# Performance work log

Measured on AMD Instinct MI355X. Metric: run time of the kernel, lower is better.

Reference implementation:

```python
import jax, jax.numpy as jnp
import numpy as np

N_INIT = jnp.array([17.047, 14.099, 3.625], dtype=jnp.float32)
CA_INIT = jnp.array([16.967, 12.784, 4.338], dtype=jnp.float32)
C_INIT = jnp.array([15.685, 12.755, 5.133], dtype=jnp.float32)


def _unit(x):
    return x / (jnp.linalg.norm(x, axis=-1, keepdims=True) + 1e-8)


def _place_dihedral(a, b, c, bond_angle, bond_length, torsion):
    # a,b,c: [B,3]; bond_angle/bond_length/torsion: [B]
    ab = b - a
    bc = _unit(c - b)
    cr = jnp.cross(ab, bc)
    crn = jnp.linalg.norm(cr, axis=-1, keepdims=True)
    n_main = _unit(cr)
    # collinear fallback (per-element; almost never triggers for real angles)
    perp = jnp.zeros_like(bc).at[..., 0].set(1.0)
    ct = jnp.cross(bc, perp)
    ctn = jnp.linalg.norm(ct, axis=-1, keepdims=True)
    perp2 = jnp.where(ctn < 1e-6, jnp.zeros_like(bc).at[..., 1].set(1.0), perp)
    n_fb = _unit(jnp.cross(bc, perp2))
    n = jnp.where(crn < 1e-6, n_fb, n_main)
    nbc = jnp.cross(n, bc)
    m = jnp.stack([bc, nbc, n], axis=-1)  # [B,3,3]
    d_local = jnp.stack([
        -bond_length * jnp.cos(bond_angle),
        bond_length * jnp.cos(torsion) * jnp.sin(bond_angle),
        bond_length * jnp.sin(torsion) * jnp.sin(bond_angle),
    ], axis=-1)  # [B,3]
    d = jnp.einsum('bij,bj->bi', m, d_local)
    return d + c


def _nerf_build(phi, psi, omega, bond_lengths, bond_angles):
    B, L = phi.shape
    init = jnp.broadcast_to(jnp.stack([N_INIT, CA_INIT, C_INIT]), (B, 3, 3))
    # per-step params, leading axis = residue index i in [0, L-2]
    xs = (
        psi[:, :L - 1].T,                 # psi_i
        omega[:, :L - 1].T,               # omega_i
        phi[:, 1:].T,                     # phi_{i+1}
        bond_lengths[:, :L - 1, 2].T,     # C-N length
        bond_lengths[:, :L - 1, 0].T,     # N-CA length
        bond_lengths[:, :L - 1, 1].T,     # CA-C length
        bond_angles[:, :L - 1, 1].T,      # CA-C-N angle
        bond_angles[:, :L - 1, 2].T,      # C-N-CA angle
        bond_angles[:, :L - 1, 0].T,      # N-CA-C angle
    )

    def step(prev, x):
        psi_i, omega_i, phi_i, len_cn, len_nca, len_cac, ang_cacn, ang_cnca, ang_ncac = x
        a, b, c = prev[:, 0], prev[:, 1], prev[:, 2]
        n = _place_dihedral(a, b, c, ang_cacn, len_cn, psi_i)
        ca = _place_dihedral(b, c, n, ang_cnca, len_nca, omega_i)
        cc = _place_dihedral(c, n, ca, ang_ncac, len_cac, phi_i)
        new = jnp.stack([n, ca, cc], axis=1)  # [B,3,3]
        return new, new

    _, outs = jax.lax.scan(step, init, xs)  # [L-1,B,3,3]
    rest = outs.transpose(1, 0, 2, 3).reshape(B, 3 * (L - 1), 3)
    return jnp.concatenate([init, rest], axis=1)  # [B, 3L, 3]


def setup_inputs() -> dict:
    key = jax.random.key(0)
    k0, k1, k2, k3, k4 = jax.random.split(key, 5)
    B, L = 4096, 512
    phi = jax.random.normal(k0, (B, L), dtype=jnp.float32)
    psi = jax.random.normal(k1, (B, L), dtype=jnp.float32)
    omega = jax.random.normal(k2, (B, L), dtype=jnp.float32)
    # realistic positive bond lengths (~1.0-1.5 A) and bond angles (~1.5-2.3 rad)
    bond_lengths = 1.0 + 0.5 * jax.random.uniform(k3, (B, L, 3), dtype=jnp.float32)
    bond_angles = 1.5 + 0.8 * jax.random.uniform(k4, (B, L, 3), dtype=jnp.float32)
    return {"phi": phi, "psi": psi, "omega": omega,
            "bond_lengths": bond_lengths, "bond_angles": bond_angles}


def reference(phi, psi, omega, bond_lengths, bond_angles):
    return _nerf_build(phi, psi, omega, bond_lengths, bond_angles)
```

## Files before the change

### kernel.cpp

```cpp
#include <hip/hip_runtime.h>
#include <math.h>


#define LCH 512
#define NRES 511
#define RPL 8

struct Xf { float r[9]; float t[3]; };

__device__ __forceinline__ Xf xf_compose(const Xf& A, const Xf& B) {
  Xf C;
#pragma unroll
  for (int i = 0; i < 3; ++i) {
    float a0 = A.r[3*i+0], a1 = A.r[3*i+1], a2 = A.r[3*i+2];
    C.r[3*i+0] = a0*B.r[0] + a1*B.r[3] + a2*B.r[6];
    C.r[3*i+1] = a0*B.r[1] + a1*B.r[4] + a2*B.r[7];
    C.r[3*i+2] = a0*B.r[2] + a1*B.r[5] + a2*B.r[8];
    C.t[i]     = a0*B.t[0] + a1*B.t[1] + a2*B.t[2] + A.t[i];
  }
  return C;
}

__device__ __forceinline__ void xf_step(Xf& P, float theta, float len, float tau) {
  float st, ct, sx, cx;
  __sincosf(theta, &st, &ct);
  __sincosf(tau, &sx, &cx);
  float ux = -ct, uy = cx*st, uz = sx*st;
  float v0 = -st, v1 = -ct*cx, v2 = -ct*sx;
  float c00 = P.r[0]*ux + P.r[1]*uy + P.r[2]*uz;
  float c10 = P.r[3]*ux + P.r[4]*uy + P.r[5]*uz;
  float c20 = P.r[6]*ux + P.r[7]*uy + P.r[8]*uz;
  float c01 = P.r[0]*v0 + P.r[1]*v1 + P.r[2]*v2;
  float c11 = P.r[3]*v0 + P.r[4]*v1 + P.r[5]*v2;
  float c21 = P.r[6]*v0 + P.r[7]*v1 + P.r[8]*v2;
  float c02 = P.r[2]*cx - P.r[1]*sx;
  float c12 = P.r[5]*cx - P.r[4]*sx;
  float c22 = P.r[8]*cx - P.r[7]*sx;
  P.t[0] += len*c00; P.t[1] += len*c10; P.t[2] += len*c20;
  P.r[0]=c00; P.r[1]=c01; P.r[2]=c02;
  P.r[3]=c10; P.r[4]=c11; P.r[5]=c12;
  P.r[6]=c20; P.r[7]=c21; P.r[8]=c22;
}

__device__ __forceinline__ void xf_set_delta(Xf& P, float theta, float len, float tau) {
  float st, ct, sx, cx;
  __sincosf(theta, &st, &ct);
  __sincosf(tau, &sx, &cx);
  float ux = -ct, uy = cx*st, uz = sx*st;
  P.r[0]=ux; P.r[1]=-st;    P.r[2]=0.f;
  P.r[3]=uy; P.r[4]=-ct*cx; P.r[5]=-sx;
  P.r[6]=uz; P.r[7]=-ct*sx; P.r[8]=cx;
  P.t[0]=len*ux; P.t[1]=len*uy; P.t[2]=len*uz;
}

__device__ __forceinline__ Xf xf_shfl_up(const Xf& P, int d) {
  Xf O;
#pragma unroll
  for (int i = 0; i < 9; ++i) O.r[i] = __shfl_up(P.r[i], d, 64);
#pragma unroll
  for (int i = 0; i < 3; ++i) O.t[i] = __shfl_up(P.t[i], d, 64);
  return O;
}

static __device__ const float c_init[9] = {
  17.047f, 14.099f, 3.625f,
  16.967f, 12.784f, 4.338f,
  15.685f, 12.755f, 5.133f };

__global__ __launch_bounds__(256) void nerf_wavescan_kernel(
    const float* __restrict__ g_phi, const float* __restrict__ g_psi,
    const float* __restrict__ g_omg, const float* __restrict__ g_bl,
    const float* __restrict__ g_ba, float* __restrict__ g_out)
{
  const int lane  = threadIdx.x & 63;
  const int wave  = threadIdx.x >> 6;
  const int chain = blockIdx.x * 4 + wave;

  const float* phir = g_phi + (size_t)chain * LCH;
  const float* psir = g_psi + (size_t)chain * LCH;
  const float* omgr = g_omg + (size_t)chain * LCH;
  const float* blr  = g_bl  + (size_t)chain * LCH * 3;
  const float* bar  = g_ba  + (size_t)chain * LCH * 3;

  const int j0 = lane * RPL;

  float psi_[RPL], omg_[RPL], phl_[RPL];
  float bl_[3*RPL], ba_[3*RPL];
  {
    const float4* p;
    p = (const float4*)(psir + j0);
#pragma unroll
    for (int q = 0; q < RPL/4; ++q) { float4 v = p[q];
      psi_[4*q]=v.x; psi_[4*q+1]=v.y; psi_[4*q+2]=v.z; psi_[4*q+3]=v.w; }
    p = (const float4*)(omgr + j0);
#pragma unroll
    for (int q = 0; q < RPL/4; ++q) { float4 v = p[q];
      omg_[4*q]=v.x; omg_[4*q+1]=v.y; omg_[4*q+2]=v.z; omg_[4*q+3]=v.w; }
    p = (const float4*)(phir + j0);
#pragma unroll
    for (int q = 0; q < RPL/4; ++q) { float4 v = p[q];
      phl_[4*q]=v.x; phl_[4*q+1]=v.y; phl_[4*q+2]=v.z; phl_[4*q+3]=v.w; }
    p = (const float4*)(blr + (size_t)j0*3);
#pragma unroll
    for (int q = 0; q < (3*RPL)/4; ++q) { float4 v = p[q];
      bl_[4*q]=v.x; bl_[4*q+1]=v.y; bl_[4*q+2]=v.z; bl_[4*q+3]=v.w; }
    p = (const float4*)(bar + (size_t)j0*3);
#pragma unroll
    for (int q = 0; q < (3*RPL)/4; ++q) { float4 v = p[q];
      ba_[4*q]=v.x; ba_[4*q+1]=v.y; ba_[4*q+2]=v.z; ba_[4*q+3]=v.w; }
  }
  float phi_next = __shfl_down(phl_[0], 1, 64);
  float phiN[RPL];
#pragma unroll
  for (int e = 0; e < RPL-1; ++e) phiN[e] = phl_[e+1];
  phiN[RPL-1] = phi_next;

  Xf P;
  xf_set_delta(P, ba_[1], bl_[2], psi_[0]);
  xf_step(P, ba_[2], bl_[0], omg_[0]);
  xf_step(P, ba_[0], bl_[1], phiN[0]);
#pragma unroll
  for (int e = 1; e < RPL; ++e) {
    if (j0 + e < NRES) {
      xf_step(P, ba_[3*e+1], bl_[3*e+2], psi_[e]);
      xf_step(P, ba_[3*e+2], bl_[3*e+0], omg_[e]);
      xf_step(P, ba_[3*e+0], bl_[3*e+1], phiN[e]);
    }
  }

#pragma unroll
  for (int d = 1; d < 64; d <<= 1) {
    Xf O = xf_shfl_up(P, d);
    if (lane >= d) P = xf_compose(O, P);
  }

  Xf E = xf_shfl_up(P, 1);
  Xf A;
  {
    const float ax=17.047f, ay=14.099f, az=3.625f;
    const float bx_=16.967f, by_=12.784f, bz_=4.338f;
    const float cx_=15.685f, cy_=12.755f, cz_=5.133f;
    float abx=bx_-ax, aby=by_-ay, abz=bz_-az;
    float vx=cx_-bx_, vy=cy_-by_, vz=cz_-bz_;
    float vn = sqrtf(vx*vx+vy*vy+vz*vz) + 1e-8f;
    vx/=vn; vy/=vn; vz/=vn;
    float crx = aby*vz - abz*vy;
    float cry = abz*vx - abx*vz;
    float crz = abx*vy - aby*vx;
    float cn = sqrtf(crx*crx+cry*cry+crz*crz) + 1e-8f;
    float nx=crx/cn, ny=cry/cn, nz=crz/cn;
    float mx = ny*vz - nz*vy;
    float my = nz*vx - nx*vz;
    float mz = nx*vy - ny*vx;
    Xf I0;
    I0.r[0]=vx; I0.r[1]=mx; I0.r[2]=nx;
    I0.r[3]=vy; I0.r[4]=my; I0.r[5]=ny;
    I0.r[6]=vz; I0.r[7]=mz; I0.r[8]=nz;
    I0.t[0]=cx_; I0.t[1]=cy_; I0.t[2]=cz_;
    A = (lane == 0) ? I0 : xf_compose(I0, E);
  }

  float* orow = g_out + (size_t)chain * (3*LCH) * 3;
  if (lane < 9) orow[lane] = c_init[lane];

#pragma unroll
  for (int e = 0; e < RPL; ++e) {
    int j = j0 + e;
    if (j < NRES) {
      float* o = orow + (size_t)(3 + 3*j) * 3;
      xf_step(A, ba_[3*e+1], bl_[3*e+2], psi_[e]);
      o[0]=A.t[0]; o[1]=A.t[1]; o[2]=A.t[2];
      xf_step(A, ba_[3*e+2], bl_[3*e+0], omg_[e]);
      o[3]=A.t[0]; o[4]=A.t[1]; o[5]=A.t[2];
      xf_step(A, ba_[3*e+0], bl_[3*e+1], phiN[e]);
      o[6]=A.t[0]; o[7]=A.t[1]; o[8]=A.t[2];
    }
  }
}

extern "C" void kernel_launch(void* const* d_in, const int* in_sizes, int n_in,
                              void* d_out, int out_size, void* d_ws, size_t ws_size,
                              hipStream_t stream) {
  const float* phi = (const float*)d_in[0];
  const float* psi = (const float*)d_in[1];
  const float* omg = (const float*)d_in[2];
  const float* bl  = (const float*)d_in[3];
  const float* ba  = (const float*)d_in[4];
  float* out = (float*)d_out;
  const int B = in_sizes[0] / LCH;
  hipLaunchKernelGGL(nerf_wavescan_kernel, dim3(B / 4), dim3(256), 0, stream,
                     phi, psi, omg, bl, ba, out);
}
```

Before: 171.5 us.

## Stage output in LDS for coalesced float4 stores; realign per-lane residue ownership

Each lane now owns output atoms 72*lane..72*lane+71 by shifting residue ownership by one, pulling the previous lane's last-residue params via shuffles, and dropping the tail bounds checks. Outputs are written to a padded per-wave shared-memory buffer (stride 73), then written back as fully coalesced float4 stores across the wave. This replaces the scattered strided 4-byte global stores. In exchange it adds LDS traffic, shuffles, some index arithmetic, and 73 KB of shared memory per block, which limits occupancy.

```diff
diff --git a/kernel.cpp b/kernel.cpp
--- a/kernel.cpp
+++ b/kernel.cpp
@@ -4,7 +4,6 @@
 
 #define LCH 512
 #define NRES 511
-#define RPL 8
 
 struct Xf { float r[9]; float t[3]; };
 
@@ -53,6 +52,13 @@
   P.t[0]=len*ux; P.t[1]=len*uy; P.t[2]=len*uz;
 }
 
+__device__ __forceinline__ void xf_identity(Xf& A) {
+  A.r[0]=1.f; A.r[1]=0.f; A.r[2]=0.f;
+  A.r[3]=0.f; A.r[4]=1.f; A.r[5]=0.f;
+  A.r[6]=0.f; A.r[7]=0.f; A.r[8]=1.f;
+  A.t[0]=0.f; A.t[1]=0.f; A.t[2]=0.f;
+}
+
 __device__ __forceinline__ Xf xf_shfl_up(const Xf& P, int d) {
   Xf O;
 #pragma unroll
@@ -62,19 +68,19 @@
   return O;
 }
 
-static __device__ const float c_init[9] = {
-  17.047f, 14.099f, 3.625f,
-  16.967f, 12.784f, 4.338f,
-  15.685f, 12.755f, 5.133f };
+#define LSTRIDE 73
 
 __global__ __launch_bounds__(256) void nerf_wavescan_kernel(
     const float* __restrict__ g_phi, const float* __restrict__ g_psi,
     const float* __restrict__ g_omg, const float* __restrict__ g_bl,
     const float* __restrict__ g_ba, float* __restrict__ g_out)
 {
+  __shared__ float S[4][LSTRIDE * 64];
+
   const int lane  = threadIdx.x & 63;
   const int wave  = threadIdx.x >> 6;
   const int chain = blockIdx.x * 4 + wave;
+  float* sw = &S[wave][0];
 
   const float* phir = g_phi + (size_t)chain * LCH;
   const float* psir = g_psi + (size_t)chain * LCH;
@@ -82,50 +88,52 @@
   const float* blr  = g_bl  + (size_t)chain * LCH * 3;
   const float* bar  = g_ba  + (size_t)chain * LCH * 3;
 
-  const int j0 = lane * RPL;
-
-  float psi_[RPL], omg_[RPL], phl_[RPL];
-  float bl_[3*RPL], ba_[3*RPL];
+  const int j0 = lane * 8;
+
+  float psi_[8], omg_[8], phl_[8], bl_[24], ba_[24];
   {
     const float4* p;
     p = (const float4*)(psir + j0);
 #pragma unroll
-    for (int q = 0; q < RPL/4; ++q) { float4 v = p[q];
+    for (int q = 0; q < 2; ++q) { float4 v = p[q];
       psi_[4*q]=v.x; psi_[4*q+1]=v.y; psi_[4*q+2]=v.z; psi_[4*q+3]=v.w; }
     p = (const float4*)(omgr + j0);
 #pragma unroll
-    for (int q = 0; q < RPL/4; ++q) { float4 v = p[q];
+    for (int q = 0; q < 2; ++q) { float4 v = p[q];
       omg_[4*q]=v.x; omg_[4*q+1]=v.y; omg_[4*q+2]=v.z; omg_[4*q+3]=v.w; }
     p = (const float4*)(phir + j0);
 #pragma unroll
-    for (int q = 0; q < RPL/4; ++q) { float4 v = p[q];
+    for (int q = 0; q < 2; ++q) { float4 v = p[q];
       phl_[4*q]=v.x; phl_[4*q+1]=v.y; phl_[4*q+2]=v.z; phl_[4*q+3]=v.w; }
     p = (const float4*)(blr + (size_t)j0*3);
 #pragma unroll
-    for (int q = 0; q < (3*RPL)/4; ++q) { float4 v = p[q];
+    for (int q = 0; q < 6; ++q) { float4 v = p[q];
       bl_[4*q]=v.x; bl_[4*q+1]=v.y; bl_[4*q+2]=v.z; bl_[4*q+3]=v.w; }
     p = (const float4*)(bar + (size_t)j0*3);
 #pragma unroll
-    for (int q = 0; q < (3*RPL)/4; ++q) { float4 v = p[q];
+    for (int q = 0; q < 6; ++q) { float4 v = p[q];
       ba_[4*q]=v.x; ba_[4*q+1]=v.y; ba_[4*q+2]=v.z; ba_[4*q+3]=v.w; }
   }
-  float phi_next = __shfl_down(phl_[0], 1, 64);
-  float phiN[RPL];
-#pragma unroll
-  for (int e = 0; e < RPL-1; ++e) phiN[e] = phl_[e+1];
-  phiN[RPL-1] = phi_next;
+
+  float psip = __shfl_up(psi_[7], 1, 64);
+  float omgp = __shfl_up(omg_[7], 1, 64);
+  float pbl0 = __shfl_up(bl_[21], 1, 64);
+  float pbl1 = __shfl_up(bl_[22], 1, 64);
+  float pbl2 = __shfl_up(bl_[23], 1, 64);
+  float pba0 = __shfl_up(ba_[21], 1, 64);
+  float pba1 = __shfl_up(ba_[22], 1, 64);
+  float pba2 = __shfl_up(ba_[23], 1, 64);
 
   Xf P;
-  xf_set_delta(P, ba_[1], bl_[2], psi_[0]);
-  xf_step(P, ba_[2], bl_[0], omg_[0]);
-  xf_step(P, ba_[0], bl_[1], phiN[0]);
-#pragma unroll
-  for (int e = 1; e < RPL; ++e) {
-    if (j0 + e < NRES) {
-      xf_step(P, ba_[3*e+1], bl_[3*e+2], psi_[e]);
-      xf_step(P, ba_[3*e+2], bl_[3*e+0], omg_[e]);
-      xf_step(P, ba_[3*e+0], bl_[3*e+1], phiN[e]);
-    }
+  xf_set_delta(P, pba1, pbl2, psip);
+  xf_step(P, pba2, pbl0, omgp);
+  xf_step(P, pba0, pbl1, phl_[0]);
+  if (lane == 0) xf_identity(P);
+#pragma unroll
+  for (int e = 0; e < 7; ++e) {
+    xf_step(P, ba_[3*e+1], bl_[3*e+2], psi_[e]);
+    xf_step(P, ba_[3*e+2], bl_[3*e+0], omg_[e]);
+    xf_step(P, ba_[3*e+0], bl_[3*e+1], phl_[e+1]);
   }
 
 #pragma unroll
@@ -160,21 +168,44 @@
     A = (lane == 0) ? I0 : xf_compose(I0, E);
   }
 
-  float* orow = g_out + (size_t)chain * (3*LCH) * 3;
-  if (lane < 9) orow[lane] = c_init[lane];
-
-#pragma unroll
-  for (int e = 0; e < RPL; ++e) {
-    int j = j0 + e;
-    if (j < NRES) {
-      float* o = orow + (size_t)(3 + 3*j) * 3;
-      xf_step(A, ba_[3*e+1], bl_[3*e+2], psi_[e]);
-      o[0]=A.t[0]; o[1]=A.t[1]; o[2]=A.t[2];
-      xf_step(A, ba_[3*e+2], bl_[3*e+0], omg_[e]);
-      o[3]=A.t[0]; o[4]=A.t[1]; o[5]=A.t[2];
-      xf_step(A, ba_[3*e+0], bl_[3*e+1], phiN[e]);
-      o[6]=A.t[0]; o[7]=A.t[1]; o[8]=A.t[2];
-    }
+  float* reg = sw + LSTRIDE * lane;
+  if (lane != 0) {
+    xf_step(A, pba1, pbl2, psip);
+    reg[0]=A.t[0]; reg[1]=A.t[1]; reg[2]=A.t[2];
+    xf_step(A, pba2, pbl0, omgp);
+    reg[3]=A.t[0]; reg[4]=A.t[1]; reg[5]=A.t[2];
+    xf_step(A, pba0, pbl1, phl_[0]);
+    reg[6]=A.t[0]; reg[7]=A.t[1]; reg[8]=A.t[2];
+  } else {
+    reg[0]=17.047f; reg[1]=14.099f; reg[2]=3.625f;
+    reg[3]=16.967f; reg[4]=12.784f; reg[5]=4.338f;
+    reg[6]=15.685f; reg[7]=12.755f; reg[8]=5.133f;
+  }
+#pragma unroll
+  for (int e = 0; e < 7; ++e) {
+    float* o = reg + 9 + 9*e;
+    xf_step(A, ba_[3*e+1], bl_[3*e+2], psi_[e]);
+    o[0]=A.t[0]; o[1]=A.t[1]; o[2]=A.t[2];
+    xf_step(A, ba_[3*e+2], bl_[3*e+0], omg_[e]);
+    o[3]=A.t[0]; o[4]=A.t[1]; o[5]=A.t[2];
+    xf_step(A, ba_[3*e+0], bl_[3*e+1], phl_[e+1]);
+    o[6]=A.t[0]; o[7]=A.t[1]; o[8]=A.t[2];
+  }
+
+  float* orow = g_out + (size_t)chain * (3 * LCH) * 3;
+  int g0 = 4 * lane;
+  int lo = g0 / 72;
+  int f  = g0 - 72 * lo;
+  int addr = LSTRIDE * lo + f;
+#pragma unroll
+  for (int q = 0; q < 18; ++q) {
+    float4 v;
+    v.x = sw[addr]; v.y = sw[addr+1]; v.z = sw[addr+2]; v.w = sw[addr+3];
+    *(float4*)(orow + 4*lane + 256*q) = v;
+    f += 40;
+    int wrap = (f >= 72) ? 1 : 0;
+    f -= 72 * wrap;
+    addr += 259 + wrap;
   }
 }
 
```

Result: faster. 167.1 us (-2.6%).

## Split each chain across a 256-thread block with two-level scan and LDS-staged output

Applied to the files above, without the earlier changes.

Each chain now gets a whole 256-thread block instead of one wave, so each thread handles two residues rather than eight. The per-wave transform totals are combined through shared memory. Outputs are staged in LDS and written back with coalesced stores instead of strided per-thread writes. This gives more parallelism and better store coalescing, at the cost of more compose work, block barriers, and less coalesced scalar input loads.

```diff
diff --git a/kernel.cpp b/kernel.cpp
--- a/kernel.cpp
+++ b/kernel.cpp
@@ -3,8 +3,6 @@
 
 
 #define LCH 512
-#define NRES 511
-#define RPL 8
 
 struct Xf { float r[9]; float t[3]; };
 
@@ -53,6 +51,13 @@
   P.t[0]=len*ux; P.t[1]=len*uy; P.t[2]=len*uz;
 }
 
+__device__ __forceinline__ void xf_identity(Xf& A) {
+  A.r[0]=1.f; A.r[1]=0.f; A.r[2]=0.f;
+  A.r[3]=0.f; A.r[4]=1.f; A.r[5]=0.f;
+  A.r[6]=0.f; A.r[7]=0.f; A.r[8]=1.f;
+  A.t[0]=0.f; A.t[1]=0.f; A.t[2]=0.f;
+}
+
 __device__ __forceinline__ Xf xf_shfl_up(const Xf& P, int d) {
   Xf O;
 #pragma unroll
@@ -62,19 +67,25 @@
   return O;
 }
 
-static __device__ const float c_init[9] = {
-  17.047f, 14.099f, 3.625f,
-  16.967f, 12.784f, 4.338f,
-  15.685f, 12.755f, 5.133f };
-
-__global__ __launch_bounds__(256) void nerf_wavescan_kernel(
+__device__ __forceinline__ void xf_load_lds(const float* p, Xf& A) {
+#pragma unroll
+  for (int i = 0; i < 9; ++i) A.r[i] = p[i];
+#pragma unroll
+  for (int i = 0; i < 3; ++i) A.t[i] = p[9+i];
+}
+
+__global__ __launch_bounds__(256) void nerf_r6_kernel(
     const float* __restrict__ g_phi, const float* __restrict__ g_psi,
     const float* __restrict__ g_omg, const float* __restrict__ g_bl,
     const float* __restrict__ g_ba, float* __restrict__ g_out)
 {
-  const int lane  = threadIdx.x & 63;
-  const int wave  = threadIdx.x >> 6;
-  const int chain = blockIdx.x * 4 + wave;
+  __shared__ float s_tot[48];
+  __shared__ float s_out[4608];
+
+  const int t    = threadIdx.x;
+  const int lane = t & 63;
+  const int wave = t >> 6;
+  const int chain = blockIdx.x;
 
   const float* phir = g_phi + (size_t)chain * LCH;
   const float* psir = g_psi + (size_t)chain * LCH;
@@ -82,51 +93,25 @@
   const float* blr  = g_bl  + (size_t)chain * LCH * 3;
   const float* bar  = g_ba  + (size_t)chain * LCH * 3;
 
-  const int j0 = lane * RPL;
-
-  float psi_[RPL], omg_[RPL], phl_[RPL];
-  float bl_[3*RPL], ba_[3*RPL];
-  {
-    const float4* p;
-    p = (const float4*)(psir + j0);
-#pragma unroll
-    for (int q = 0; q < RPL/4; ++q) { float4 v = p[q];
-      psi_[4*q]=v.x; psi_[4*q+1]=v.y; psi_[4*q+2]=v.z; psi_[4*q+3]=v.w; }
-    p = (const float4*)(omgr + j0);
-#pragma unroll
-    for (int q = 0; q < RPL/4; ++q) { float4 v = p[q];
-      omg_[4*q]=v.x; omg_[4*q+1]=v.y; omg_[4*q+2]=v.z; omg_[4*q+3]=v.w; }
-    p = (const float4*)(phir + j0);
-#pragma unroll
-    for (int q = 0; q < RPL/4; ++q) { float4 v = p[q];
-      phl_[4*q]=v.x; phl_[4*q+1]=v.y; phl_[4*q+2]=v.z; phl_[4*q+3]=v.w; }
-    p = (const float4*)(blr + (size_t)j0*3);
-#pragma unroll
-    for (int q = 0; q < (3*RPL)/4; ++q) { float4 v = p[q];
-      bl_[4*q]=v.x; bl_[4*q+1]=v.y; bl_[4*q+2]=v.z; bl_[4*q+3]=v.w; }
-    p = (const float4*)(bar + (size_t)j0*3);
-#pragma unroll
-    for (int q = 0; q < (3*RPL)/4; ++q) { float4 v = p[q];
-      ba_[4*q]=v.x; ba_[4*q+1]=v.y; ba_[4*q+2]=v.z; ba_[4*q+3]=v.w; }
-  }
-  float phi_next = __shfl_down(phl_[0], 1, 64);
-  float phiN[RPL];
-#pragma unroll
-  for (int e = 0; e < RPL-1; ++e) phiN[e] = phl_[e+1];
-  phiN[RPL-1] = phi_next;
+  const int jm = (2*t - 1) > 0 ? (2*t - 1) : 0;
+  const int jo = 2*t;
+
+  float psiA = psir[jm], psiB = psir[jo];
+  float omgA = omgr[jm], omgB = omgr[jo];
+  float phiA = phir[jo], phiB = phir[jo + 1];
+  float blA0 = blr[3*jm+0], blA1 = blr[3*jm+1], blA2 = blr[3*jm+2];
+  float blB0 = blr[3*jo+0], blB1 = blr[3*jo+1], blB2 = blr[3*jo+2];
+  float baA0 = bar[3*jm+0], baA1 = bar[3*jm+1], baA2 = bar[3*jm+2];
+  float baB0 = bar[3*jo+0], baB1 = bar[3*jo+1], baB2 = bar[3*jo+2];
 
   Xf P;
-  xf_set_delta(P, ba_[1], bl_[2], psi_[0]);
-  xf_step(P, ba_[2], bl_[0], omg_[0]);
-  xf_step(P, ba_[0], bl_[1], phiN[0]);
-#pragma unroll
-  for (int e = 1; e < RPL; ++e) {
-    if (j0 + e < NRES) {
-      xf_step(P, ba_[3*e+1], bl_[3*e+2], psi_[e]);
-      xf_step(P, ba_[3*e+2], bl_[3*e+0], omg_[e]);
-      xf_step(P, ba_[3*e+0], bl_[3*e+1], phiN[e]);
-    }
-  }
+  xf_set_delta(P, baA1, blA2, psiA);
+  xf_step(P, baA2, blA0, omgA);
+  xf_step(P, baA0, blA1, phiA);
+  if (t == 0) xf_identity(P);
+  xf_step(P, baB1, blB2, psiB);
+  xf_step(P, baB2, blB0, omgB);
+  xf_step(P, baB0, blB1, phiB);
 
 #pragma unroll
   for (int d = 1; d < 64; d <<= 1) {
@@ -134,7 +119,15 @@
     if (lane >= d) P = xf_compose(O, P);
   }
 
+  if (lane == 63) {
+#pragma unroll
+    for (int i = 0; i < 9; ++i) s_tot[12*wave + i] = P.r[i];
+#pragma unroll
+    for (int i = 0; i < 3; ++i) s_tot[12*wave + 9 + i] = P.t[i];
+  }
   Xf E = xf_shfl_up(P, 1);
+  __syncthreads();
+
   Xf A;
   {
     const float ax=17.047f, ay=14.099f, az=3.625f;
@@ -152,29 +145,45 @@
     float mx = ny*vz - nz*vy;
     float my = nz*vx - nx*vz;
     float mz = nx*vy - ny*vx;
-    Xf I0;
-    I0.r[0]=vx; I0.r[1]=mx; I0.r[2]=nx;
-    I0.r[3]=vy; I0.r[4]=my; I0.r[5]=ny;
-    I0.r[6]=vz; I0.r[7]=mz; I0.r[8]=nz;
-    I0.t[0]=cx_; I0.t[1]=cy_; I0.t[2]=cz_;
-    A = (lane == 0) ? I0 : xf_compose(I0, E);
-  }
-
-  float* orow = g_out + (size_t)chain * (3*LCH) * 3;
-  if (lane < 9) orow[lane] = c_init[lane];
-
-#pragma unroll
-  for (int e = 0; e < RPL; ++e) {
-    int j = j0 + e;
-    if (j < NRES) {
-      float* o = orow + (size_t)(3 + 3*j) * 3;
-      xf_step(A, ba_[3*e+1], bl_[3*e+2], psi_[e]);
-      o[0]=A.t[0]; o[1]=A.t[1]; o[2]=A.t[2];
-      xf_step(A, ba_[3*e+2], bl_[3*e+0], omg_[e]);
-      o[3]=A.t[0]; o[4]=A.t[1]; o[5]=A.t[2];
-      xf_step(A, ba_[3*e+0], bl_[3*e+1], phiN[e]);
-      o[6]=A.t[0]; o[7]=A.t[1]; o[8]=A.t[2];
-    }
+    A.r[0]=vx; A.r[1]=mx; A.r[2]=nx;
+    A.r[3]=vy; A.r[4]=my; A.r[5]=ny;
+    A.r[6]=vz; A.r[7]=mz; A.r[8]=nz;
+    A.t[0]=cx_; A.t[1]=cy_; A.t[2]=cz_;
+  }
+  if (wave >= 1) { Xf T; xf_load_lds(&s_tot[0],  T); A = xf_compose(A, T); }
+  if (wave >= 2) { Xf T; xf_load_lds(&s_tot[12], T); A = xf_compose(A, T); }
+  if (wave >= 3) { Xf T; xf_load_lds(&s_tot[24], T); A = xf_compose(A, T); }
+  if (lane > 0) A = xf_compose(A, E);
+
+  float* o = s_out + 18 * t;
+  if (t == 0) {
+    o[0]=17.047f; o[1]=14.099f; o[2]=3.625f;
+    o[3]=16.967f; o[4]=12.784f; o[5]=4.338f;
+    o[6]=15.685f; o[7]=12.755f; o[8]=5.133f;
+  } else {
+    xf_step(A, baA1, blA2, psiA);
+    o[0]=A.t[0]; o[1]=A.t[1]; o[2]=A.t[2];
+    xf_step(A, baA2, blA0, omgA);
+    o[3]=A.t[0]; o[4]=A.t[1]; o[5]=A.t[2];
+    xf_step(A, baA0, blA1, phiA);
+    o[6]=A.t[0]; o[7]=A.t[1]; o[8]=A.t[2];
+  }
+  xf_step(A, baB1, blB2, psiB);
+  o[9]=A.t[0];  o[10]=A.t[1]; o[11]=A.t[2];
+  xf_step(A, baB2, blB0, omgB);
+  o[12]=A.t[0]; o[13]=A.t[1]; o[14]=A.t[2];
+  xf_step(A, baB0, blB1, phiB);
+  o[15]=A.t[0]; o[16]=A.t[1]; o[17]=A.t[2];
+  __syncthreads();
+
+  float* orow = g_out + (size_t)chain * 4608;
+#pragma unroll
+  for (int q = 0; q < 9; ++q) {
+    int g = 2*t + 512*q;
+    float x = s_out[g];
+    float y = s_out[g + 1];
+    orow[g]     = x;
+    orow[g + 1] = y;
   }
 }
 
@@ -188,6 +197,6 @@
   const float* ba  = (const float*)d_in[4];
   float* out = (float*)d_out;
   const int B = in_sizes[0] / LCH;
-  hipLaunchKernelGGL(nerf_wavescan_kernel, dim3(B / 4), dim3(256), 0, stream,
+  hipLaunchKernelGGL(nerf_r6_kernel, dim3(B), dim3(256), 0, stream,
                      phi, psi, omg, bl, ba, out);
 }
```

New measurement: 146.1 us. 14.8% less time.
